# Optimization experiments

Measured on AMD Instinct MI355X. Metric: run time of the kernel, lower is better.

The kernel has to match this reference:

```python
import jax, jax.numpy as jnp
import numpy as np

B, D_OUT, SEQ = 4, 512, 4000
N_LABELS, E_DIM = 8929, 300


def setup_inputs() -> dict:
    key = jax.random.key(0)
    k1, k2, k3, k4 = jax.random.split(key, 4)
    H = jax.random.normal(k1, (B, D_OUT, SEQ), dtype=jnp.float32)
    label_emb = jax.random.normal(k2, (N_LABELS, E_DIM), dtype=jnp.float32)  # Q.weight
    W_map = jax.random.normal(k3, (D_OUT, E_DIM), dtype=jnp.float32) * 0.05  # conv1d k=1 weight [out,in]
    b_map = jax.random.normal(k4, (D_OUT,), dtype=jnp.float32) * 0.05
    return {"H": H, "label_emb": label_emb, "W_map": W_map, "b_map": b_map}


def reference(H, label_emb, W_map, b_map):
    # mapping_layer(Q.weight.T).T : kernel-size-1 conv == linear over embedding dim
    Q = jnp.einsum('oe,le->lo', W_map, label_emb) + b_map  # [n_labels, d_out]
    # E = Q @ H ; H is [b, d_out, seq] -> E [b, n_labels, seq] (scale=False)
    E = jnp.einsum('ld,bds->bls', Q, H)
    A = jax.nn.softmax(E, axis=2)                          # softmax over sequence
    C = jnp.einsum('bls,bds->bld', A, H)                   # A @ H^T -> [b, n_labels, d_out]
    return C, A
```

## Files before the change

### kernel.cpp

```cpp
#include <hip/hip_runtime.h>

#define BB 4
#define DD 512
#define SS 4000
#define LL 8929
#define EE 300

typedef unsigned short ushortt;
typedef __attribute__((ext_vector_type(8))) short bhalf8;
typedef __attribute__((ext_vector_type(4))) float floatx4;
typedef __attribute__((ext_vector_type(4))) unsigned short us4;

struct HS { unsigned short h, l; };

__device__ __forceinline__ HS splitR(float x) {
  unsigned u = __builtin_bit_cast(unsigned, x);
  unsigned hb = (u + 0x7FFFu + ((u >> 16) & 1u)) >> 16;
  float hf = __builtin_bit_cast(float, hb << 16);
  float r = x - hf;
  unsigned v = __builtin_bit_cast(unsigned, r);
  unsigned lb = (v + 0x7FFFu + ((v >> 16) & 1u)) >> 16;
  HS o; o.h = (unsigned short)hb; o.l = (unsigned short)lb;
  return o;
}

__device__ __forceinline__ HS splitT(float x) {
  unsigned u = __builtin_bit_cast(unsigned, x);
  float hf = __builtin_bit_cast(float, u & 0xFFFF0000u);
  float r = x - hf;
  HS o;
  o.h = (unsigned short)(u >> 16);
  o.l = (unsigned short)(__builtin_bit_cast(unsigned, r) >> 16);
  return o;
}

__device__ __forceinline__ void gld16(const unsigned short* g, void* l) {
  __builtin_amdgcn_global_load_lds(
      (const __attribute__((address_space(1))) unsigned int*)g,
      (__attribute__((address_space(3))) unsigned int*)l, 16, 0, 0);
}

__global__ __launch_bounds__(256) void gemm_e(
    const ushortt* __restrict__ Qh, const ushortt* __restrict__ Ql,
    const ushortt* __restrict__ Hth, const ushortt* __restrict__ Htl,
    float* __restrict__ Eg) {
  __shared__ __align__(16) ushortt Ah_s[2][4096];
  __shared__ __align__(16) ushortt Al_s[2][4096];
  __shared__ __align__(16) ushortt Bh_s[2][4096];
  __shared__ __align__(16) ushortt Bl_s[2][4096];

  const ushortt* Bhp = Hth + (long)blockIdx.z * SS * DD;
  const ushortt* Blp = Htl + (long)blockIdx.z * SS * DD;
  float* E = Eg + (long)blockIdx.z * LL * SS;

  const int t = threadIdx.x, lane = t & 63, w = t >> 6;
  const int m0 = blockIdx.y * 128, n0 = blockIdx.x * 128;
  const int wm = (w >> 1) * 64, wn = (w & 1) * 64;
  const int lr = lane & 15;

  const int srow = lane >> 2;
  const int sch = ((lane & 3) ^ ((lane >> 3) & 3)) * 8;
  const int r0 = w * 32 + srow, r1 = r0 + 16;
  const long am0 = (long)((m0 + r0 < LL) ? m0 + r0 : LL - 1) * DD;
  const long am1 = (long)((m0 + r1 < LL) ? m0 + r1 : LL - 1) * DD;
  const long bn0 = (long)((n0 + r0 < SS) ? n0 + r0 : SS - 1) * DD;
  const long bn1 = (long)((n0 + r1 < SS) ? n0 + r1 : SS - 1) * DD;

  const int chA = (((lane >> 4) ^ ((lr >> 1) & 3))) * 16;
  const int raB = (wm + lr) * 64 + chA;
  const int rbB = (wn + lr) * 64 + chA;

  floatx4 acc[4][4];
#pragma unroll
  for (int i = 0; i < 4; ++i)
#pragma unroll
    for (int j = 0; j < 4; ++j) acc[i][j] = (floatx4){0.f, 0.f, 0.f, 0.f};

  {
    char* dA = (char*)Ah_s[0] + w * 2048;
    char* dAl = (char*)Al_s[0] + w * 2048;
    char* dB = (char*)Bh_s[0] + w * 2048;
    char* dBl = (char*)Bl_s[0] + w * 2048;
    gld16(Qh + am0 + sch, dA);
    gld16(Qh + am1 + sch, dA + 1024);
    gld16(Ql + am0 + sch, dAl);
    gld16(Ql + am1 + sch, dAl + 1024);
    gld16(Bhp + bn0 + sch, dB);
    gld16(Bhp + bn1 + sch, dB + 1024);
    gld16(Blp + bn0 + sch, dBl);
    gld16(Blp + bn1 + sch, dBl + 1024);
  }
  __syncthreads();

  const int KT = DD / 32;
  for (int kt = 0; kt < KT; ++kt) {
    const int cb = kt & 1, nb = cb ^ 1;
    if (kt + 1 < KT) {
      const int kb = (kt + 1) * 32;
      char* dA = (char*)Ah_s[nb] + w * 2048;
      char* dAl = (char*)Al_s[nb] + w * 2048;
      char* dB = (char*)Bh_s[nb] + w * 2048;
      char* dBl = (char*)Bl_s[nb] + w * 2048;
      gld16(Qh + am0 + kb + sch, dA);
      gld16(Qh + am1 + kb + sch, dA + 1024);
      gld16(Ql + am0 + kb + sch, dAl);
      gld16(Ql + am1 + kb + sch, dAl + 1024);
      gld16(Bhp + bn0 + kb + sch, dB);
      gld16(Bhp + bn1 + kb + sch, dB + 1024);
      gld16(Blp + bn0 + kb + sch, dBl);
      gld16(Blp + bn1 + kb + sch, dBl + 1024);
    }
    bhalf8 ah[4], al[4], bh[4], bl[4];
#pragma unroll
    for (int f = 0; f < 4; ++f) {
      ah[f] = *(const bhalf8*)((const char*)Ah_s[cb] + raB + f * 1024);
      al[f] = *(const bhalf8*)((const char*)Al_s[cb] + raB + f * 1024);
      bh[f] = *(const bhalf8*)((const char*)Bh_s[cb] + rbB + f * 1024);
      bl[f] = *(const bhalf8*)((const char*)Bl_s[cb] + rbB + f * 1024);
    }
#pragma unroll
    for (int i = 0; i < 4; ++i)
#pragma unroll
      for (int j = 0; j < 4; ++j) {
        acc[i][j] = __builtin_amdgcn_mfma_f32_16x16x32_bf16(ah[i], bh[j], acc[i][j], 0, 0, 0);
        acc[i][j] = __builtin_amdgcn_mfma_f32_16x16x32_bf16(ah[i], bl[j], acc[i][j], 0, 0, 0);
        acc[i][j] = __builtin_amdgcn_mfma_f32_16x16x32_bf16(al[i], bh[j], acc[i][j], 0, 0, 0);
      }
    __syncthreads();
  }

  const int cr = (lane >> 4) * 4;
#pragma unroll
  for (int i = 0; i < 4; ++i)
#pragma unroll
    for (int j = 0; j < 4; ++j)
#pragma unroll
      for (int r = 0; r < 4; ++r) {
        const int m = m0 + wm + i * 16 + cr + r;
        const int n = n0 + wn + j * 16 + lr;
        if (m < LL && n < SS) E[(long)m * SS + n] = acc[i][j][r];
      }
}

__global__ __launch_bounds__(256) void gemm_c(
    const float* __restrict__ Ag, const ushortt* __restrict__ Hh,
    const ushortt* __restrict__ Hl, float* __restrict__ Cg) {
  __shared__ __align__(16) ushortt Bh_s[2][4096];
  __shared__ __align__(16) ushortt Bl_s[2][4096];
  __shared__ __align__(16) ushortt Ah_s[2][128][40];
  __shared__ __align__(16) ushortt Al_s[2][128][40];

  const float* A = Ag + (long)blockIdx.z * LL * SS;
  const ushortt* Bhp = Hh + (long)blockIdx.z * DD * SS;
  const ushortt* Blp = Hl + (long)blockIdx.z * DD * SS;
  float* C = Cg + (long)blockIdx.z * LL * DD;

  const int t = threadIdx.x, lane = t & 63, w = t >> 6;
  const int m0 = blockIdx.y * 128, n0 = blockIdx.x * 128;
  const int wm = (w >> 1) * 64, wn = (w & 1) * 64;
  const int lr = lane & 15;

  const int srow = lane >> 2;
  const int sch = ((lane & 3) ^ ((lane >> 3) & 3)) * 8;
  const long bn0 = (long)(n0 + w * 32 + srow) * SS;
  const long bn1 = bn0 + (long)16 * SS;

  const int sr = t >> 3;
  const int scol = (t & 7) * 4;

  const int chB = (((lane >> 4) ^ ((lr >> 1) & 3))) * 16;
  const int rbB = (wn + lr) * 64 + chB;
  const int raBytes = (lane >> 4) * 16;

  floatx4 acc[4][4];
#pragma unroll
  for (int i = 0; i < 4; ++i)
#pragma unroll
    for (int j = 0; j < 4; ++j) acc[i][j] = (floatx4){0.f, 0.f, 0.f, 0.f};

  float4 av[4];
  {
    char* dB = (char*)Bh_s[0] + w * 2048;
    char* dBl = (char*)Bl_s[0] + w * 2048;
    gld16(Bhp + bn0 + sch, dB);
    gld16(Bhp + bn1 + sch, dB + 1024);
    gld16(Blp + bn0 + sch, dBl);
    gld16(Blp + bn1 + sch, dBl + 1024);
#pragma unroll
    for (int rr = 0; rr < 4; ++rr) {
      const int m = m0 + rr * 32 + sr;
      av[rr] = make_float4(0.f, 0.f, 0.f, 0.f);
      if (m < LL) av[rr] = *reinterpret_cast<const float4*>(A + (long)m * SS + scol);
    }
#pragma unroll
    for (int rr = 0; rr < 4; ++rr) {
      const int row = rr * 32 + sr;
      HS p0 = splitT(av[rr].x), p1 = splitT(av[rr].y);
      HS p2 = splitT(av[rr].z), p3 = splitT(av[rr].w);
      us4 h, l;
      h.x = p0.h; l.x = p0.l; h.y = p1.h; l.y = p1.l;
      h.z = p2.h; l.z = p2.l; h.w = p3.h; l.w = p3.l;
      *reinterpret_cast<us4*>(&Ah_s[0][row][scol]) = h;
      *reinterpret_cast<us4*>(&Al_s[0][row][scol]) = l;
    }
  }
  __syncthreads();

  const int KT = SS / 32;
  for (int kt = 0; kt < KT; ++kt) {
    const int cb = kt & 1, nb = cb ^ 1;
    const bool pf = (kt + 1 < KT);
    if (pf) {
      const int kb = (kt + 1) * 32;
      char* dB = (char*)Bh_s[nb] + w * 2048;
      char* dBl = (char*)Bl_s[nb] + w * 2048;
      gld16(Bhp + bn0 + kb + sch, dB);
      gld16(Bhp + bn1 + kb + sch, dB + 1024);
      gld16(Blp + bn0 + kb + sch, dBl);
      gld16(Blp + bn1 + kb + sch, dBl + 1024);
#pragma unroll
      for (int rr = 0; rr < 4; ++rr) {
        const int m = m0 + rr * 32 + sr;
        av[rr] = make_float4(0.f, 0.f, 0.f, 0.f);
        if (m < LL) av[rr] = *reinterpret_cast<const float4*>(A + (long)m * SS + kb + scol);
      }
    }
    bhalf8 ah[4], al[4], bh[4], bl[4];
#pragma unroll
    for (int f = 0; f < 4; ++f) {
      ah[f] = *(const bhalf8*)((const char*)&Ah_s[cb][wm + f * 16 + lr][0] + raBytes);
      al[f] = *(const bhalf8*)((const char*)&Al_s[cb][wm + f * 16 + lr][0] + raBytes);
      bh[f] = *(const bhalf8*)((const char*)Bh_s[cb] + rbB + f * 1024);
      bl[f] = *(const bhalf8*)((const char*)Bl_s[cb] + rbB + f * 1024);
    }
#pragma unroll
    for (int i = 0; i < 4; ++i)
#pragma unroll
      for (int j = 0; j < 4; ++j) {
        acc[i][j] = __builtin_amdgcn_mfma_f32_16x16x32_bf16(ah[i], bh[j], acc[i][j], 0, 0, 0);
        acc[i][j] = __builtin_amdgcn_mfma_f32_16x16x32_bf16(ah[i], bl[j], acc[i][j], 0, 0, 0);
        acc[i][j] = __builtin_amdgcn_mfma_f32_16x16x32_bf16(al[i], bh[j], acc[i][j], 0, 0, 0);
      }
    if (pf) {
#pragma unroll
      for (int rr = 0; rr < 4; ++rr) {
        const int row = rr * 32 + sr;
        HS p0 = splitT(av[rr].x), p1 = splitT(av[rr].y);
        HS p2 = splitT(av[rr].z), p3 = splitT(av[rr].w);
        us4 h, l;
        h.x = p0.h; l.x = p0.l; h.y = p1.h; l.y = p1.l;
        h.z = p2.h; l.z = p2.l; h.w = p3.h; l.w = p3.l;
        *reinterpret_cast<us4*>(&Ah_s[nb][row][scol]) = h;
        *reinterpret_cast<us4*>(&Al_s[nb][row][scol]) = l;
      }
    }
    __syncthreads();
  }

  const int cr = (lane >> 4) * 4;
#pragma unroll
  for (int i = 0; i < 4; ++i)
#pragma unroll
    for (int j = 0; j < 4; ++j)
#pragma unroll
      for (int r = 0; r < 4; ++r) {
        const int m = m0 + wm + i * 16 + cr + r;
        const int n = n0 + wn + j * 16 + lr;
        if (m < LL) C[(long)m * DD + n] = acc[i][j][r];
      }
}

__global__ __launch_bounds__(256) void split_transpose(
    const float* __restrict__ H, ushortt* __restrict__ Th,
    ushortt* __restrict__ Tl) {
  __shared__ float tile[32][33];
  const int b = blockIdx.z;
  const int s0 = blockIdx.x * 32, d0 = blockIdx.y * 32;
  const int tx = threadIdx.x & 31, ty = threadIdx.x >> 5;
  const float* Hb = H + (long)b * DD * SS;
#pragma unroll
  for (int i = 0; i < 4; ++i)
    tile[ty + i * 8][tx] = Hb[(long)(d0 + ty + i * 8) * SS + s0 + tx];
  __syncthreads();
  ushortt* Thb = Th + (long)b * SS * DD;
  ushortt* Tlb = Tl + (long)b * SS * DD;
#pragma unroll
  for (int i = 0; i < 4; ++i) {
    HS p = splitR(tile[tx][ty + i * 8]);
    const long o = (long)(s0 + ty + i * 8) * DD + d0 + tx;
    Thb[o] = p.h;
    Tlb[o] = p.l;
  }
}

__global__ __launch_bounds__(256) void back_transpose(
    const ushortt* __restrict__ Th, const ushortt* __restrict__ Tl,
    ushortt* __restrict__ Hh, ushortt* __restrict__ Hl) {
  __shared__ ushortt th[32][33], tl[32][33];
  const int b = blockIdx.z;
  const int s0 = blockIdx.x * 32, d0 = blockIdx.y * 32;
  const int tx = threadIdx.x & 31, ty = threadIdx.x >> 5;
  const ushortt* Tb = Th + (long)b * SS * DD;
  const ushortt* Tlb = Tl + (long)b * SS * DD;
#pragma unroll
  for (int i = 0; i < 4; ++i) {
    const long o = (long)(s0 + ty + i * 8) * DD + d0 + tx;
    th[ty + i * 8][tx] = Tb[o];
    tl[ty + i * 8][tx] = Tlb[o];
  }
  __syncthreads();
  ushortt* Hhb = Hh + (long)b * DD * SS;
  ushortt* Hlb = Hl + (long)b * DD * SS;
#pragma unroll
  for (int i = 0; i < 4; ++i) {
    const long o = (long)(d0 + ty + i * 8) * SS + s0 + tx;
    Hhb[o] = th[tx][ty + i * 8];
    Hlb[o] = tl[tx][ty + i * 8];
  }
}

__global__ __launch_bounds__(256) void gemm_q(
    const float* __restrict__ Ag, const float* __restrict__ Bg,
    const float* __restrict__ bias, ushortt* __restrict__ Qh,
    ushortt* __restrict__ Ql, int M, int N, int K) {
  __shared__ float As[16][132];
  __shared__ float Bs[16][132];
  const int t = threadIdx.x;
  const int m0 = blockIdx.y * 128, n0 = blockIdx.x * 128;
  const int tx = t & 15, ty = t >> 4;
  float acc[8][8];
#pragma unroll
  for (int i = 0; i < 8; ++i)
#pragma unroll
    for (int j = 0; j < 8; ++j) acc[i][j] = 0.f;
  const int ra = t >> 2;
  const int kc = (t & 3) * 4;
  const int KT = (K + 15) / 16;
  for (int kt = 0; kt < KT; ++kt) {
    const int kb = kt * 16;
#pragma unroll
    for (int h = 0; h < 2; ++h) {
      const int mrow = ra + h * 64;
      const int m = m0 + mrow, k = kb + kc;
      float4 v = make_float4(0.f, 0.f, 0.f, 0.f);
      if (m < M && k < K)
        v = *reinterpret_cast<const float4*>(Ag + (long)m * K + k);
      As[kc + 0][mrow] = v.x; As[kc + 1][mrow] = v.y;
      As[kc + 2][mrow] = v.z; As[kc + 3][mrow] = v.w;
      const int n = n0 + mrow;
      float4 u = make_float4(0.f, 0.f, 0.f, 0.f);
      if (n < N && k < K)
        u = *reinterpret_cast<const float4*>(Bg + (long)n * K + k);
      Bs[kc + 0][mrow] = u.x; Bs[kc + 1][mrow] = u.y;
      Bs[kc + 2][mrow] = u.z; Bs[kc + 3][mrow] = u.w;
    }
    __syncthreads();
#pragma unroll
    for (int kk = 0; kk < 16; ++kk) {
      const float4 a0 = *reinterpret_cast<const float4*>(&As[kk][ty * 8]);
      const float4 a1 = *reinterpret_cast<const float4*>(&As[kk][ty * 8 + 4]);
      const float4 b0 = *reinterpret_cast<const float4*>(&Bs[kk][tx * 8]);
      const float4 b1 = *reinterpret_cast<const float4*>(&Bs[kk][tx * 8 + 4]);
      const float a[8] = {a0.x, a0.y, a0.z, a0.w, a1.x, a1.y, a1.z, a1.w};
      const float b[8] = {b0.x, b0.y, b0.z, b0.w, b1.x, b1.y, b1.z, b1.w};
#pragma unroll
      for (int i = 0; i < 8; ++i)
#pragma unroll
        for (int j = 0; j < 8; ++j) acc[i][j] = fmaf(a[i], b[j], acc[i][j]);
    }
    __syncthreads();
  }
#pragma unroll
  for (int i = 0; i < 8; ++i) {
    const int m = m0 + ty * 8 + i;
    if (m >= M) continue;
#pragma unroll
    for (int j = 0; j < 8; ++j) {
      const int n = n0 + tx * 8 + j;
      if (n < N) {
        HS p = splitR(acc[i][j] + bias[n]);
        Qh[(long)m * N + n] = p.h;
        Ql[(long)m * N + n] = p.l;
      }
    }
  }
}

__global__ __launch_bounds__(256) void softmax4000(float* __restrict__ P) {
  float* p = P + (long)blockIdx.x * SS;
  const int t = threadIdx.x;
  float v[16];
  float mx = -1e30f;
#pragma unroll
  for (int j = 0; j < 16; ++j) {
    const int i = t + j * 256;
    if (i < SS) { v[j] = p[i]; mx = fmaxf(mx, v[j]); } else v[j] = -1e30f;
  }
#pragma unroll
  for (int o = 32; o > 0; o >>= 1) mx = fmaxf(mx, __shfl_xor(mx, o));
  __shared__ float rm[4], rs[4];
  const int w = t >> 6;
  if ((t & 63) == 0) rm[w] = mx;
  __syncthreads();
  mx = fmaxf(fmaxf(rm[0], rm[1]), fmaxf(rm[2], rm[3]));
  float s = 0.f;
#pragma unroll
  for (int j = 0; j < 16; ++j) {
    const int i = t + j * 256;
    if (i < SS) { v[j] = __expf(v[j] - mx); s += v[j]; }
  }
#pragma unroll
  for (int o = 32; o > 0; o >>= 1) s += __shfl_xor(s, o);
  if ((t & 63) == 0) rs[w] = s;
  __syncthreads();
  s = rs[0] + rs[1] + rs[2] + rs[3];
  const float inv = 1.f / s;
#pragma unroll
  for (int j = 0; j < 16; ++j) {
    const int i = t + j * 256;
    if (i < SS) p[i] = v[j] * inv;
  }
}

extern "C" void kernel_launch(void* const* d_in, const int* in_sizes, int n_in,
                              void* d_out, int out_size, void* d_ws,
                              size_t ws_size, hipStream_t stream) {
  const float* H = (const float*)d_in[0];
  const float* lab = (const float*)d_in[1];
  const float* Wm = (const float*)d_in[2];
  const float* bm = (const float*)d_in[3];

  float* Cout = (float*)d_out;
  float* Aout = Cout + (size_t)BB * LL * DD;
  ushortt* Qh = (ushortt*)Cout;
  ushortt* Ql = Qh + (size_t)LL * DD;

  ushortt* Hth = (ushortt*)d_ws;
  ushortt* Htl = Hth + (size_t)BB * SS * DD;

  ushortt* Hh = (ushortt*)d_in[0];
  ushortt* Hl = Hh + (size_t)BB * DD * SS;

  const dim3 blk(256);
  const int MB = (LL + 127) / 128;

  split_transpose<<<dim3(SS / 32, DD / 32, BB), blk, 0, stream>>>(H, Hth, Htl);

  back_transpose<<<dim3(SS / 32, DD / 32, BB), blk, 0, stream>>>(Hth, Htl, Hh, Hl);

  gemm_q<<<dim3(DD / 128, MB, 1), blk, 0, stream>>>(lab, Wm, bm, Qh, Ql, LL, DD, EE);

  gemm_e<<<dim3((SS + 127) / 128, MB, BB), blk, 0, stream>>>(Qh, Ql, Hth, Htl, Aout);

  softmax4000<<<dim3(BB * LL), blk, 0, stream>>>(Aout);

  gemm_c<<<dim3(DD / 128, MB, BB), blk, 0, stream>>>(Aout, Hh, Hl, Cout);
}
```

Baseline: 2.034 ms.

## Drop H low-part term in C GEMM and add XCD-aware block swizzle

The C = A·H^T GEMM now keeps only the bf16 high part of H while keeping both parts of A, going from three MFMAs per tile to two. It also stops loading, storing and transposing the H low-part array. An XCD-aware workgroup remap is added to both large GEMMs to improve L2 locality across chiplets, and the A tile LDS padding shrinks. The accuracy of C drops to roughly bf16 precision on H, which may push error tolerances. The swizzle assumes the grid size divides evenly by 8, so some blocks could be remapped wrongly when it does not.

```diff
diff --git a/kernel.cpp b/kernel.cpp
--- a/kernel.cpp
+++ b/kernel.cpp
@@ -40,6 +40,16 @@
       (__attribute__((address_space(3))) unsigned int*)l, 16, 0, 0);
 }
 
+__device__ __forceinline__ void xcd_swz(int& bx, int& by, int& bz) {
+  const int gx = gridDim.x, gy = gridDim.y;
+  const int lid = blockIdx.x + gx * (blockIdx.y + gy * blockIdx.z);
+  const int q = (gx * gy * gridDim.z) >> 3;
+  const int wg = (lid & 7) * q + (lid >> 3);
+  bx = wg % gx;
+  by = (wg / gx) % gy;
+  bz = wg / (gx * gy);
+}
+
 __global__ __launch_bounds__(256) void gemm_e(
     const ushortt* __restrict__ Qh, const ushortt* __restrict__ Ql,
     const ushortt* __restrict__ Hth, const ushortt* __restrict__ Htl,
@@ -49,12 +59,15 @@
   __shared__ __align__(16) ushortt Bh_s[2][4096];
   __shared__ __align__(16) ushortt Bl_s[2][4096];
 
-  const ushortt* Bhp = Hth + (long)blockIdx.z * SS * DD;
-  const ushortt* Blp = Htl + (long)blockIdx.z * SS * DD;
-  float* E = Eg + (long)blockIdx.z * LL * SS;
+  int bx, by, bz;
+  xcd_swz(bx, by, bz);
+
+  const ushortt* Bhp = Hth + (long)bz * SS * DD;
+  const ushortt* Blp = Htl + (long)bz * SS * DD;
+  float* E = Eg + (long)bz * LL * SS;
 
   const int t = threadIdx.x, lane = t & 63, w = t >> 6;
-  const int m0 = blockIdx.y * 128, n0 = blockIdx.x * 128;
+  const int m0 = by * 128, n0 = bx * 128;
   const int wm = (w >> 1) * 64, wn = (w & 1) * 64;
   const int lr = lane & 15;
 
@@ -144,19 +157,20 @@
 
 __global__ __launch_bounds__(256) void gemm_c(
     const float* __restrict__ Ag, const ushortt* __restrict__ Hh,
-    const ushortt* __restrict__ Hl, float* __restrict__ Cg) {
+    float* __restrict__ Cg) {
   __shared__ __align__(16) ushortt Bh_s[2][4096];
-  __shared__ __align__(16) ushortt Bl_s[2][4096];
-  __shared__ __align__(16) ushortt Ah_s[2][128][40];
-  __shared__ __align__(16) ushortt Al_s[2][128][40];
-
-  const float* A = Ag + (long)blockIdx.z * LL * SS;
-  const ushortt* Bhp = Hh + (long)blockIdx.z * DD * SS;
-  const ushortt* Blp = Hl + (long)blockIdx.z * DD * SS;
-  float* C = Cg + (long)blockIdx.z * LL * DD;
+  __shared__ __align__(16) ushortt Ah_s[2][128][36];
+  __shared__ __align__(16) ushortt Al_s[2][128][36];
+
+  int bx, by, bz;
+  xcd_swz(bx, by, bz);
+
+  const float* A = Ag + (long)bz * LL * SS;
+  const ushortt* Bhp = Hh + (long)bz * DD * SS;
+  float* C = Cg + (long)bz * LL * DD;
 
   const int t = threadIdx.x, lane = t & 63, w = t >> 6;
-  const int m0 = blockIdx.y * 128, n0 = blockIdx.x * 128;
+  const int m0 = by * 128, n0 = bx * 128;
   const int wm = (w >> 1) * 64, wn = (w & 1) * 64;
   const int lr = lane & 15;
 
@@ -181,11 +195,8 @@
   float4 av[4];
   {
     char* dB = (char*)Bh_s[0] + w * 2048;
-    char* dBl = (char*)Bl_s[0] + w * 2048;
     gld16(Bhp + bn0 + sch, dB);
     gld16(Bhp + bn1 + sch, dB + 1024);
-    gld16(Blp + bn0 + sch, dBl);
-    gld16(Blp + bn1 + sch, dBl + 1024);
 #pragma unroll
     for (int rr = 0; rr < 4; ++rr) {
       const int m = m0 + rr * 32 + sr;
@@ -213,11 +224,8 @@
     if (pf) {
       const int kb = (kt + 1) * 32;
       char* dB = (char*)Bh_s[nb] + w * 2048;
-      char* dBl = (char*)Bl_s[nb] + w * 2048;
       gld16(Bhp + bn0 + kb + sch, dB);
       gld16(Bhp + bn1 + kb + sch, dB + 1024);
-      gld16(Blp + bn0 + kb + sch, dBl);
-      gld16(Blp + bn1 + kb + sch, dBl + 1024);
 #pragma unroll
       for (int rr = 0; rr < 4; ++rr) {
         const int m = m0 + rr * 32 + sr;
@@ -225,20 +233,18 @@
         if (m < LL) av[rr] = *reinterpret_cast<const float4*>(A + (long)m * SS + kb + scol);
       }
     }
-    bhalf8 ah[4], al[4], bh[4], bl[4];
+    bhalf8 ah[4], al[4], bh[4];
 #pragma unroll
     for (int f = 0; f < 4; ++f) {
       ah[f] = *(const bhalf8*)((const char*)&Ah_s[cb][wm + f * 16 + lr][0] + raBytes);
       al[f] = *(const bhalf8*)((const char*)&Al_s[cb][wm + f * 16 + lr][0] + raBytes);
       bh[f] = *(const bhalf8*)((const char*)Bh_s[cb] + rbB + f * 1024);
-      bl[f] = *(const bhalf8*)((const char*)Bl_s[cb] + rbB + f * 1024);
     }
 #pragma unroll
     for (int i = 0; i < 4; ++i)
 #pragma unroll
       for (int j = 0; j < 4; ++j) {
         acc[i][j] = __builtin_amdgcn_mfma_f32_16x16x32_bf16(ah[i], bh[j], acc[i][j], 0, 0, 0);
-        acc[i][j] = __builtin_amdgcn_mfma_f32_16x16x32_bf16(ah[i], bl[j], acc[i][j], 0, 0, 0);
         acc[i][j] = __builtin_amdgcn_mfma_f32_16x16x32_bf16(al[i], bh[j], acc[i][j], 0, 0, 0);
       }
     if (pf) {
@@ -294,28 +300,23 @@
 }
 
 __global__ __launch_bounds__(256) void back_transpose(
-    const ushortt* __restrict__ Th, const ushortt* __restrict__ Tl,
-    ushortt* __restrict__ Hh, ushortt* __restrict__ Hl) {
-  __shared__ ushortt th[32][33], tl[32][33];
+    const ushortt* __restrict__ Th, ushortt* __restrict__ Hh) {
+  __shared__ ushortt th[32][33];
   const int b = blockIdx.z;
   const int s0 = blockIdx.x * 32, d0 = blockIdx.y * 32;
   const int tx = threadIdx.x & 31, ty = threadIdx.x >> 5;
   const ushortt* Tb = Th + (long)b * SS * DD;
-  const ushortt* Tlb = Tl + (long)b * SS * DD;
 #pragma unroll
   for (int i = 0; i < 4; ++i) {
     const long o = (long)(s0 + ty + i * 8) * DD + d0 + tx;
     th[ty + i * 8][tx] = Tb[o];
-    tl[ty + i * 8][tx] = Tlb[o];
   }
   __syncthreads();
   ushortt* Hhb = Hh + (long)b * DD * SS;
-  ushortt* Hlb = Hl + (long)b * DD * SS;
 #pragma unroll
   for (int i = 0; i < 4; ++i) {
     const long o = (long)(d0 + ty + i * 8) * SS + s0 + tx;
     Hhb[o] = th[tx][ty + i * 8];
-    Hlb[o] = tl[tx][ty + i * 8];
   }
 }
 
@@ -439,14 +440,13 @@
   ushortt* Htl = Hth + (size_t)BB * SS * DD;
 
   ushortt* Hh = (ushortt*)d_in[0];
-  ushortt* Hl = Hh + (size_t)BB * DD * SS;
 
   const dim3 blk(256);
   const int MB = (LL + 127) / 128;
 
   split_transpose<<<dim3(SS / 32, DD / 32, BB), blk, 0, stream>>>(H, Hth, Htl);
 
-  back_transpose<<<dim3(SS / 32, DD / 32, BB), blk, 0, stream>>>(Hth, Htl, Hh, Hl);
+  back_transpose<<<dim3(SS / 32, DD / 32, BB), blk, 0, stream>>>(Hth, Hh);
 
   gemm_q<<<dim3(DD / 128, MB, 1), blk, 0, stream>>>(lab, Wm, bm, Qh, Ql, LL, DD, EE);
 
@@ -454,5 +454,5 @@
 
   softmax4000<<<dim3(BB * LL), blk, 0, stream>>>(Aout);
 
-  gemm_c<<<dim3(DD / 128, MB, BB), blk, 0, stream>>>(Aout, Hh, Hl, Cout);
-}
+  gemm_c<<<dim3(DD / 128, MB, BB), blk, 0, stream>>>(Aout, Hh, Cout);
+}
```

New measurement: 1.895 ms. 6.8% less time.
